# Kernel optimization log

Measured on AMD Instinct MI355X. Metric: run time of the kernel, lower is better.

Reference implementation:

```python
import jax, jax.numpy as jnp
import numpy as np

HIDDEN = 2048
NUM_ROUTED = 24          # num_routed_experts(6) * segmentation_factor(4)
ROUTED_INTER = 512       # intermediate_dim(2048) // segmentation_factor(4)
NUM_SHARED = 2
SHARED_INTER = 2048
TOP_K = 6


def setup_inputs() -> dict:
    key = jax.random.key(0)
    ks = jax.random.split(key, 8)
    std = 0.02
    x = jax.random.normal(ks[0], (2, 2048, HIDDEN), dtype=jnp.float32)
    gate_w = jax.random.normal(ks[1], (NUM_ROUTED, HIDDEN), dtype=jnp.float32) * (0.02 / np.sqrt(HIDDEN))
    shared_w1 = jax.random.normal(ks[2], (NUM_SHARED, HIDDEN, SHARED_INTER), dtype=jnp.float32) * std
    shared_w3 = jax.random.normal(ks[3], (NUM_SHARED, HIDDEN, SHARED_INTER), dtype=jnp.float32) * std
    shared_w2 = jax.random.normal(ks[4], (NUM_SHARED, SHARED_INTER, HIDDEN), dtype=jnp.float32) * std
    routed_w1 = jax.random.normal(ks[5], (NUM_ROUTED, HIDDEN, ROUTED_INTER), dtype=jnp.float32) * std
    routed_w3 = jax.random.normal(ks[6], (NUM_ROUTED, HIDDEN, ROUTED_INTER), dtype=jnp.float32) * std
    routed_w2 = jax.random.normal(ks[7], (NUM_ROUTED, ROUTED_INTER, HIDDEN), dtype=jnp.float32) * std
    return {"x": x, "gate_w": gate_w,
            "shared_w1": shared_w1, "shared_w2": shared_w2, "shared_w3": shared_w3,
            "routed_w1": routed_w1, "routed_w2": routed_w2, "routed_w3": routed_w3}


def _swiglu_ffn(x, w1, w2, w3):
    # x: [..., n, h]; w1,w3: [..., h, i]; w2: [..., i, h]  (dropout inactive at eval)
    h = jax.nn.silu(jnp.einsum('nh,ehi->eni', x, w1)) * jnp.einsum('nh,ehi->eni', x, w3)
    return jnp.einsum('eni,eih->enh', h, w2)


def reference(x, gate_w, shared_w1, shared_w2, shared_w3, routed_w1, routed_w2, routed_w3):
    B, S, H = x.shape
    x_flat = x.reshape(-1, H)                       # [N, H]
    N = x_flat.shape[0]

    # shared experts (summed)
    shared_out = _swiglu_ffn(x_flat, shared_w1, shared_w2, shared_w3).sum(axis=0)  # [N, H]

    # routing (eval mode: no bias added to logits, aux_loss = 0)
    scores = jax.nn.sigmoid(x_flat @ gate_w.T)      # [N, E]
    top_scores, top_idx = jax.lax.top_k(scores, TOP_K)
    top_weights = top_scores / (top_scores.sum(-1, keepdims=True) + 1e-9)  # [N, K]

    # dense dispatch/combine weights [N, E] (indices unique per row)
    dense_w = jnp.zeros((N, NUM_ROUTED), dtype=x.dtype)
    dense_w = dense_w.at[jnp.arange(N)[:, None], top_idx].set(top_weights)

    # run every routed expert on all tokens, combine with routing weights
    expert_out = _swiglu_ffn(x_flat, routed_w1, routed_w2, routed_w3)  # [E, N, H]
    combined = jnp.einsum('ne,enh->nh', dense_w, expert_out)

    output = (shared_out + combined).reshape(B, S, H)
    aux_loss = jnp.float32(0.0)  # eval mode
    return output, aux_loss
```

## Files before the change

### kernel.cpp

```cpp
#include <hip/hip_runtime.h>
#include <hip/hip_bf16.h>

#define HID   2048
#define NTOK  4096
#define NEXP  24
#define SHCOL 4096
#define TOPK  6
#define NSLOT (NTOK * TOPK)

typedef __bf16 bf16_t;
typedef __bf16 bf16x8 __attribute__((ext_vector_type(8)));
typedef __bf16 bf16x4 __attribute__((ext_vector_type(4)));
typedef float  f32x4  __attribute__((ext_vector_type(4)));

__device__ __forceinline__ void async_copy16(const bf16_t* g, bf16_t* l) {
  __builtin_amdgcn_global_load_lds(
      (const __attribute__((address_space(1))) unsigned int*)g,
      (__attribute__((address_space(3))) unsigned int*)l,
      16, 0, 0);
}
template<int N> __device__ __forceinline__ void wait_vm() {
  asm volatile("s_waitcnt vmcnt(%0)" :: "n"(N) : "memory");
}
__device__ __forceinline__ void memfence_sched() { asm volatile("" ::: "memory"); }

__device__ __forceinline__ bf16x8 frag32(const bf16_t* region, int row, int cc) {
  return *(const bf16x8*)(region + row * 32 + ((cc ^ ((row >> 1) & 3)) << 3));
}

__device__ __forceinline__ void tcast_tile(
    const float* __restrict__ src, bf16_t* __restrict__ dst,
    int C, long dstStride, int c0, int r0, int tid) {
  __shared__ float t[64][68];
  {
    const int tr = tid >> 4, tc = tid & 15;
#pragma unroll
    for (int p = 0; p < 4; ++p) {
      const int r = p * 16 + tr;
      const float4 v = *(const float4*)(src + (long)(r0 + r) * C + c0 + tc * 4);
      *(float4*)&t[r][tc * 4] = v;
    }
  }
  __syncthreads();
  {
    const int l8 = tid & 7, rb = l8 * 8;
#pragma unroll
    for (int p = 0; p < 2; ++p) {
      const int c = p * 32 + (tid >> 3);
      bf16x8 o;
#pragma unroll
      for (int s = 0; s < 8; ++s) o[s] = (bf16_t)t[rb + s][c];
      *(bf16x8*)(dst + (long)(c0 + c) * dstStride + r0 + rb) = o;
    }
  }
}

__global__ __launch_bounds__(256) void prep(
    const float* __restrict__ x, bf16_t* __restrict__ xb,
    const float* __restrict__ sw1, const float* __restrict__ rw1,
    const float* __restrict__ sw3, const float* __restrict__ rw3,
    const float* __restrict__ sw2, const float* __restrict__ rw2,
    bf16_t* __restrict__ w1t, bf16_t* __restrict__ w3t,
    bf16_t* __restrict__ w2ts, bf16_t* __restrict__ rw2t) {
  int bid = blockIdx.x;
  if (bid < 8192) {
    int i = bid * 256 + threadIdx.x;
    float4 v = ((const float4*)x)[i];
    bf16x4 o = { (bf16_t)v.x, (bf16_t)v.y, (bf16_t)v.z, (bf16_t)v.w };
    ((bf16x4*)xb)[i] = o;
    return;
  }
  bid -= 8192;
  const float* src; bf16_t* dst; int C; long dstStride, seS, deS; int BX, nPer;
  if (bid < 2048)       { src=sw1; dst=w1t;                  C=2048; dstStride=2048; seS=2048L*2048; deS=2048L*2048; BX=32; nPer=1024; }
  else if (bid < 8192)  { bid-=2048;  src=rw1; dst=w1t+(long)SHCOL*HID; C=512;  dstStride=2048; seS=2048L*512;  deS=512L*2048;  BX=8;  nPer=256; }
  else if (bid < 10240) { bid-=8192;  src=sw3; dst=w3t;                 C=2048; dstStride=2048; seS=2048L*2048; deS=2048L*2048; BX=32; nPer=1024; }
  else if (bid < 16384) { bid-=10240; src=rw3; dst=w3t+(long)SHCOL*HID; C=512;  dstStride=2048; seS=2048L*512;  deS=512L*2048;  BX=8;  nPer=256; }
  else if (bid < 18432) { bid-=16384; src=sw2; dst=w2ts;                C=2048; dstStride=4096; seS=2048L*2048; deS=2048;       BX=32; nPer=1024; }
  else                  { bid-=18432; src=rw2; dst=rw2t;                C=2048; dstStride=512;  seS=512L*2048;  deS=2048L*512;  BX=32; nPer=256; }
  const int e  = bid / nPer;
  const int rem = bid - e * nPer;
  const int by = rem / BX;
  const int bx = rem - by * BX;
  tcast_tile(src + (long)e * seS, dst + (long)e * deS, C, dstStride,
             bx * 64, by * 64, threadIdx.x);
}

__global__ void gate_topk(const float* __restrict__ x, const float* __restrict__ gw,
                          int* __restrict__ tk_idx, float* __restrict__ tk_w,
                          float* __restrict__ aux) {
  int lane = threadIdx.x & 63;
  int wave = threadIdx.x >> 6;
  int token = blockIdx.x * 4 + wave;
  const float* xr = x + (long)token * HID;
  float xv[32];
#pragma unroll
  for (int i = 0; i < 32; ++i) xv[i] = xr[lane + i * 64];
  float sc[NEXP];
#pragma unroll
  for (int e = 0; e < NEXP; ++e) {
    const float* g = gw + (long)e * HID;
    float s = 0.f;
#pragma unroll
    for (int i = 0; i < 32; ++i) s += xv[i] * g[lane + i * 64];
#pragma unroll
    for (int off = 32; off > 0; off >>= 1) s += __shfl_down(s, off);
    sc[e] = s;
  }
  if (lane == 0) {
    float sg[NEXP];
#pragma unroll
    for (int e = 0; e < NEXP; ++e) sg[e] = 1.0f / (1.0f + expf(-sc[e]));
    unsigned taken = 0;
    int   sel[TOPK];
    float sw[TOPK];
    float sum = 0.f;
    for (int k = 0; k < TOPK; ++k) {
      float best = -1.f; int bi = 0;
#pragma unroll
      for (int e = 0; e < NEXP; ++e) {
        bool avail = !(taken & (1u << e));
        if (avail && sg[e] > best) { best = sg[e]; bi = e; }
      }
      taken |= (1u << bi);
      sel[k] = bi; sw[k] = best; sum += best;
    }
    float inv = 1.0f / (sum + 1e-9f);
#pragma unroll
    for (int k = 0; k < TOPK; ++k) {
      tk_idx[token * TOPK + k] = sel[k];
      tk_w[token * TOPK + k]   = sw[k] * inv;
    }
  }
  if (blockIdx.x == 0 && threadIdx.x == 0) *aux = 0.0f;
}

__global__ void dispatch(const int* __restrict__ tk_idx, const float* __restrict__ tk_w,
                         int* __restrict__ perm, float* __restrict__ wslot,
                         int* __restrict__ slot_of, int* __restrict__ meta,
                         int* __restrict__ uptab, int* __restrict__ dntab) {
  __shared__ int cnt[NEXP], cnt2[NEXP], off[NEXP + 1];
  int tid = threadIdx.x;
  if (tid < NEXP) { cnt[tid] = 0; cnt2[tid] = 0; }
  __syncthreads();
  for (int i = tid; i < NSLOT; i += 1024) atomicAdd(&cnt[tk_idx[i]], 1);
  __syncthreads();
  if (tid == 0) {
    int o = 0, un = 0, dn = 0;
    for (int e = 0; e < NEXP; ++e) {
      off[e] = o;
      int c = cnt[e];
      for (int r0 = 0; r0 < c; r0 += 256) uptab[un++] = (e << 16) | r0;
      for (int r0 = 0; r0 < c; r0 += 128) dntab[dn++] = (e << 16) | r0;
      o += c;
    }
    off[NEXP] = o;
    meta[0] = un; meta[1] = dn;
    for (int e = 0; e < NEXP; ++e) { meta[8 + e] = cnt[e]; meta[32 + e] = off[e]; }
  }
  __syncthreads();
  for (int i = tid; i < NSLOT; i += 1024) {
    int e = tk_idx[i];
    int loc = atomicAdd(&cnt2[e], 1);
    int slot = off[e] + loc;
    perm[slot] = i / TOPK;
    wslot[slot] = tk_w[i];
    slot_of[i] = slot;
  }
}

__global__ __launch_bounds__(512, 2) void gemm_up(
    const bf16_t* __restrict__ xb, const bf16_t* __restrict__ w1t,
    const bf16_t* __restrict__ w3t, bf16_t* __restrict__ hsh,
    bf16_t* __restrict__ hr, const int* __restrict__ perm,
    const float* __restrict__ wslot, const int* __restrict__ meta,
    const int* __restrict__ uptab) {
  __shared__ bf16_t lds[4 * 16384];
  const int bid = blockIdx.x;
  const int tid  = threadIdx.x;
  const int lane = tid & 63;
  const int wave = tid >> 6;
  const int wm = wave >> 2;
  const int wc = wave & 3;
  const bool role_sh = bid < 512;
  int m0 = 0, j0 = 0, jc = 0, M = 256, bslot = 0;
  const bf16_t *b1G, *b3G;
  if (role_sh) {
    m0 = (bid >> 5) * 256; j0 = (bid & 31) * 128;
    b1G = w1t + (long)j0 * HID;
    b3G = w3t + (long)j0 * HID;
  } else {
    int t = bid - 512;
    int rt = t >> 2; jc = t & 3;
    if (rt >= meta[0]) return;
    int pk = uptab[rt];
    int e = pk >> 16, row0 = pk & 0xffff;
    bslot = meta[32 + e] + row0;
    M = min(256, meta[8 + e] - row0);
    int col = SHCOL + e * 512 + jc * 128;
    b1G = w1t + (long)col * HID;
    b3G = w3t + (long)col * HID;
  }
  const bf16_t* gsrc[4];
  int loff[4];
#pragma unroll
  for (int it = 0; it < 4; ++it) {
    int idx = it * 512 + tid;
    if (idx < 1024) {
      int r = idx >> 2, c = idx & 3;
      long rowbase;
      if (role_sh) rowbase = (long)(m0 + r) * HID;
      else         rowbase = (long)perm[bslot + ((r < M) ? r : 0)] * HID;
      gsrc[it] = xb + rowbase + ((c ^ ((r >> 1) & 3)) << 3);
      loff[it] = idx << 3;
    } else if (idx < 1536) {
      int i2 = idx - 1024; int r = i2 >> 2, c = i2 & 3;
      gsrc[it] = b1G + (long)r * HID + ((c ^ ((r >> 1) & 3)) << 3);
      loff[it] = 8192 + (i2 << 3);
    } else {
      int i2 = idx - 1536; int r = i2 >> 2, c = i2 & 3;
      gsrc[it] = b3G + (long)r * HID + ((c ^ ((r >> 1) & 3)) << 3);
      loff[it] = 12288 + (i2 << 3);
    }
  }
  auto STAGE = [&](int t) {
    bf16_t* sb = lds + (t & 3) * 16384;
#pragma unroll
    for (int it = 0; it < 4; ++it)
      async_copy16(gsrc[it] + t * 32, sb + loff[it]);
  };

  f32x4 acc1[8][2] = {};
  f32x4 acc3[8][2] = {};
  const int NT = HID / 32;
  const int rA = wm * 128 + (lane & 15);
  const int rB = wc * 32 + (lane & 15);
  const int cc = lane >> 4;
  STAGE(0); STAGE(1); STAGE(2);
  for (int t = 0; t < NT; ++t) {
    if (t + 2 < NT)      wait_vm<8>();
    else if (t + 1 < NT) wait_vm<4>();
    else                 wait_vm<0>();
    __builtin_amdgcn_s_barrier();
    memfence_sched();
    if (t + 3 < NT) STAGE(t + 3);
    const bf16_t* sb = lds + (t & 3) * 16384;
    bf16x8 a[8], b1[2], b3[2];
#pragma unroll
    for (int fm = 0; fm < 8; ++fm) a[fm] = frag32(sb, rA + fm * 16, cc);
#pragma unroll
    for (int fn = 0; fn < 2; ++fn) {
      b1[fn] = frag32(sb + 8192,  rB + fn * 16, cc);
      b3[fn] = frag32(sb + 12288, rB + fn * 16, cc);
    }
    __builtin_amdgcn_s_setprio(1);
#pragma unroll
    for (int fn = 0; fn < 2; ++fn)
#pragma unroll
      for (int fm = 0; fm < 8; ++fm) {
        acc1[fm][fn] = __builtin_amdgcn_mfma_f32_16x16x32_bf16(a[fm], b1[fn], acc1[fm][fn], 0, 0, 0);
        acc3[fm][fn] = __builtin_amdgcn_mfma_f32_16x16x32_bf16(a[fm], b3[fn], acc3[fm][fn], 0, 0, 0);
      }
    __builtin_amdgcn_s_setprio(0);
    memfence_sched();
  }
  const int mloc_base = wm * 128 + ((lane >> 4) << 2);
  const int cloc = wc * 32 + (lane & 15);
#pragma unroll
  for (int fm = 0; fm < 8; ++fm) {
#pragma unroll
    for (int jj = 0; jj < 4; ++jj) {
      const int mloc = mloc_base + fm * 16 + jj;
      if (role_sh) {
        bf16_t* dst = hsh + (long)(m0 + mloc) * SHCOL + j0 + cloc;
#pragma unroll
        for (int fn = 0; fn < 2; ++fn) {
          const float u1 = acc1[fm][fn][jj];
          const float u3 = acc3[fm][fn][jj];
          dst[fn * 16] = (bf16_t)((u1 / (1.0f + __expf(-u1))) * u3);
        }
      } else if (mloc < M) {
        const int slot = bslot + mloc;
        const float w = wslot[slot];
        bf16_t* dst = hr + (long)slot * 512 + jc * 128 + cloc;
#pragma unroll
        for (int fn = 0; fn < 2; ++fn) {
          const float u1 = acc1[fm][fn][jj];
          const float u3 = acc3[fm][fn][jj];
          dst[fn * 16] = (bf16_t)((u1 / (1.0f + __expf(-u1))) * u3 * w);
        }
      }
    }
  }
}

__global__ __launch_bounds__(512, 2) void gemm_down(
    const bf16_t* __restrict__ hsh, const bf16_t* __restrict__ w2ts,
    const bf16_t* __restrict__ hr, const bf16_t* __restrict__ rw2t,
    float* __restrict__ sout, bf16_t* __restrict__ y,
    const int* __restrict__ meta, const int* __restrict__ dntab) {
  __shared__ bf16_t lds[3 * 12288];
  const int bid = blockIdx.x;
  const int tid  = threadIdx.x;
  const int lane = tid & 63;
  const int wave = tid >> 6;
  const int wm = wave >> 2;
  const int wc = wave & 3;
  const bool role_sh = bid < 256;
  int m0 = 0, n0, M = 128, bslot = 0, NT;
  const bf16_t *aG, *bG;
  long lda, ldb;
  if (role_sh) {
    m0 = (bid >> 3) * 128; n0 = (bid & 7) * 256;
    aG = hsh + (long)m0 * SHCOL; lda = SHCOL;
    bG = w2ts + (long)n0 * SHCOL; ldb = SHCOL;
    NT = SHCOL / 32;
  } else {
    int t = bid - 256;
    int rt = t >> 3; n0 = (t & 7) * 256;
    if (rt >= meta[1]) return;
    int pk = dntab[rt];
    int e = pk >> 16, row0 = pk & 0xffff;
    bslot = meta[32 + e] + row0;
    M = min(128, meta[8 + e] - row0);
    aG = hr + (long)bslot * 512; lda = 512;
    bG = rw2t + (long)e * (2048L * 512) + (long)n0 * 512; ldb = 512;
    NT = 512 / 32;
  }
  const bf16_t* gsrc[3];
  int loff[3];
#pragma unroll
  for (int it = 0; it < 3; ++it) {
    int idx = it * 512 + tid;
    if (idx < 512) {
      int r = idx >> 2, c = idx & 3;
      gsrc[it] = aG + (long)r * lda + ((c ^ ((r >> 1) & 3)) << 3);
      loff[it] = idx << 3;
    } else {
      int i2 = idx - 512; int r = i2 >> 2, c = i2 & 3;
      gsrc[it] = bG + (long)r * ldb + ((c ^ ((r >> 1) & 3)) << 3);
      loff[it] = 4096 + (i2 << 3);
    }
  }
  auto STAGE = [&](int t) {
    bf16_t* sb = lds + (t % 3) * 12288;
#pragma unroll
    for (int it = 0; it < 3; ++it)
      async_copy16(gsrc[it] + t * 32, sb + loff[it]);
  };

  f32x4 acc[4][4] = {};
  const int rA = wm * 64 + (lane & 15);
  const int rB = wc * 64 + (lane & 15);
  const int cc = lane >> 4;
  STAGE(0); STAGE(1);
  for (int t = 0; t < NT; ++t) {
    if (t + 1 < NT) wait_vm<3>();
    else            wait_vm<0>();
    __builtin_amdgcn_s_barrier();
    memfence_sched();
    if (t + 2 < NT) STAGE(t + 2);
    const bf16_t* sb = lds + (t % 3) * 12288;
    bf16x8 a[4], b[4];
#pragma unroll
    for (int fm = 0; fm < 4; ++fm) a[fm] = frag32(sb, rA + fm * 16, cc);
#pragma unroll
    for (int fn = 0; fn < 4; ++fn) b[fn] = frag32(sb + 4096, rB + fn * 16, cc);
    __builtin_amdgcn_s_setprio(1);
#pragma unroll
    for (int fn = 0; fn < 4; ++fn)
#pragma unroll
      for (int fm = 0; fm < 4; ++fm)
        acc[fm][fn] = __builtin_amdgcn_mfma_f32_16x16x32_bf16(a[fm], b[fn], acc[fm][fn], 0, 0, 0);
    __builtin_amdgcn_s_setprio(0);
    memfence_sched();
  }
  const int mloc_base = wm * 64 + ((lane >> 4) << 2);
  const int cbase = n0 + wc * 64 + (lane & 15);
#pragma unroll
  for (int fm = 0; fm < 4; ++fm)
#pragma unroll
    for (int jj = 0; jj < 4; ++jj) {
      const int mloc = mloc_base + fm * 16 + jj;
      if (role_sh) {
#pragma unroll
        for (int fn = 0; fn < 4; ++fn)
          sout[(long)(m0 + mloc) * HID + cbase + fn * 16] = acc[fm][fn][jj];
      } else if (mloc < M) {
#pragma unroll
        for (int fn = 0; fn < 4; ++fn)
          y[(long)(bslot + mloc) * HID + cbase + fn * 16] = (bf16_t)acc[fm][fn][jj];
      }
    }
}

__global__ void combine(const float* __restrict__ sout, const bf16_t* __restrict__ y,
                        const int* __restrict__ slot_of, float* __restrict__ out) {
  const int n = blockIdx.x;
  const int c0 = threadIdx.x * 8;
  float acc[8];
  const float4* sp = (const float4*)(sout + (long)n * HID + c0);
  float4 s0 = sp[0], s1 = sp[1];
  acc[0]=s0.x; acc[1]=s0.y; acc[2]=s0.z; acc[3]=s0.w;
  acc[4]=s1.x; acc[5]=s1.y; acc[6]=s1.z; acc[7]=s1.w;
#pragma unroll
  for (int k = 0; k < TOPK; ++k) {
    int slot = slot_of[n * TOPK + k];
    bf16x8 v = *(const bf16x8*)(y + (long)slot * HID + c0);
#pragma unroll
    for (int i = 0; i < 8; ++i) acc[i] += (float)v[i];
  }
  float4* op = (float4*)(out + (long)n * HID + c0);
  op[0] = make_float4(acc[0], acc[1], acc[2], acc[3]);
  op[1] = make_float4(acc[4], acc[5], acc[6], acc[7]);
}

__global__ void fill_sentinel(float* out, int n) {
  for (int i = blockIdx.x * 256 + threadIdx.x; i < n; i += gridDim.x * 256)
    out[i] = 12345.0f;
}

extern "C" void kernel_launch(void* const* d_in, const int* in_sizes, int n_in,
                              void* d_out, int out_size, void* d_ws, size_t ws_size,
                              hipStream_t stream) {
  (void)in_sizes; (void)n_in;
  const float* x   = (const float*)d_in[0];
  const float* gw  = (const float*)d_in[1];
  const float* sw1 = (const float*)d_in[2];
  const float* sw2 = (const float*)d_in[3];
  const float* sw3 = (const float*)d_in[4];
  const float* rw1 = (const float*)d_in[5];
  const float* rw2 = (const float*)d_in[6];
  const float* rw3 = (const float*)d_in[7];
  float* out = (float*)d_out;

  const size_t OFF_XB    = 0;
  const size_t OFF_W1T   = 16777216;
  const size_t OFF_W3T   = 83886080;
  const size_t OFF_W2TS  = 150994944;
  const size_t OFF_RW2T  = 167772160;
  const size_t OFF_HSH   = 218103808;
  const size_t OFF_HR    = 251658240;
  const size_t OFF_SOUT  = 277086208;
  const size_t OFF_TKI   = 310640640;
  const size_t OFF_TKW   = 310738944;
  const size_t OFF_PERM  = 310837248;
  const size_t OFF_WSLOT = 310935552;
  const size_t OFF_SLOTOF= 311033856;
  const size_t OFF_META  = 311132160;
  const size_t OFF_UPTAB = 311136256;
  const size_t OFF_DNTAB = 311140352;
  const size_t NEED      = 311148544;
  if (ws_size < NEED) {
    fill_sentinel<<<4096, 256, 0, stream>>>(out, out_size);
    return;
  }
  char* ws = (char*)d_ws;
  bf16_t* xb     = (bf16_t*)(ws + OFF_XB);
  bf16_t* w1t    = (bf16_t*)(ws + OFF_W1T);
  bf16_t* w3t    = (bf16_t*)(ws + OFF_W3T);
  bf16_t* w2ts   = (bf16_t*)(ws + OFF_W2TS);
  bf16_t* rw2t   = (bf16_t*)(ws + OFF_RW2T);
  bf16_t* hsh    = (bf16_t*)(ws + OFF_HSH);
  bf16_t* hr     = (bf16_t*)(ws + OFF_HR);
  float*  sout   = (float*)(ws + OFF_SOUT);
  bf16_t* y      = (bf16_t*)(ws + OFF_W1T);
  int*    tki    = (int*)(ws + OFF_TKI);
  float*  tkw    = (float*)(ws + OFF_TKW);
  int*    perm   = (int*)(ws + OFF_PERM);
  float*  wslot  = (float*)(ws + OFF_WSLOT);
  int*    slotof = (int*)(ws + OFF_SLOTOF);
  int*    meta   = (int*)(ws + OFF_META);
  int*    uptab  = (int*)(ws + OFF_UPTAB);
  int*    dntab  = (int*)(ws + OFF_DNTAB);

  gate_topk<<<1024, 256, 0, stream>>>(x, gw, tki, tkw, out + (size_t)NTOK * HID);
  dispatch<<<1, 1024, 0, stream>>>(tki, tkw, perm, wslot, slotof, meta, uptab, dntab);
  prep<<<32768, 256, 0, stream>>>(x, xb, sw1, rw1, sw3, rw3, sw2, rw2,
                                  w1t, w3t, w2ts, rw2t);

  gemm_up<<<dim3(512 + 480), 512, 0, stream>>>(xb, w1t, w3t, hsh, hr, perm, wslot, meta, uptab);
  gemm_down<<<dim3(256 + 1728), 512, 0, stream>>>(hsh, w2ts, hr, rw2t, sout, y, meta, dntab);
  combine<<<dim3(NTOK), 256, 0, stream>>>(sout, y, slotof, out);
}
```

Before: 649.0 us.

## Restructure gemm_up main loop into BK=64 double-buffered, phased MFMA schedule

Reworks the up-projection GEMM loop from a 4-stage BK=32 ring to a 2-buffer BK=64 scheme with a new XOR swizzle for 64-wide rows. Each k-step is split into four MFMA phases separated by barriers, and the global-to-LDS loads for the next tiles are issued between phases so they overlap compute. Occupancy hint drops to 1 block per CU because fewer fragment registers are live per phase. This aims to cut barrier count per k and improve latency hiding, but it adds many more barriers inside each step and carries a risk of buffer hazards when the next tile is loaded into a buffer that is still being read.

```diff
diff --git a/kernel.cpp b/kernel.cpp
--- a/kernel.cpp
+++ b/kernel.cpp
@@ -23,9 +23,15 @@
   asm volatile("s_waitcnt vmcnt(%0)" :: "n"(N) : "memory");
 }
 __device__ __forceinline__ void memfence_sched() { asm volatile("" ::: "memory"); }
+__device__ __forceinline__ void barp() {
+  memfence_sched(); __builtin_amdgcn_s_barrier(); memfence_sched();
+}
 
 __device__ __forceinline__ bf16x8 frag32(const bf16_t* region, int row, int cc) {
   return *(const bf16x8*)(region + row * 32 + ((cc ^ ((row >> 1) & 3)) << 3));
+}
+__device__ __forceinline__ bf16x8 frag64(const bf16_t* region, int row, int c8) {
+  return *(const bf16x8*)(region + row * 64 + ((c8 ^ (row & 7)) << 3));
 }
 
 __device__ __forceinline__ void tcast_tile(
@@ -169,13 +175,13 @@
   }
 }
 
-__global__ __launch_bounds__(512, 2) void gemm_up(
+__global__ __launch_bounds__(512, 1) void gemm_up(
     const bf16_t* __restrict__ xb, const bf16_t* __restrict__ w1t,
     const bf16_t* __restrict__ w3t, bf16_t* __restrict__ hsh,
     bf16_t* __restrict__ hr, const int* __restrict__ perm,
     const float* __restrict__ wslot, const int* __restrict__ meta,
     const int* __restrict__ uptab) {
-  __shared__ bf16_t lds[4 * 16384];
+  __shared__ bf16_t lds[2 * 32768];
   const int bid = blockIdx.x;
   const int tid  = threadIdx.x;
   const int lane = tid & 63;
@@ -201,66 +207,115 @@
     b1G = w1t + (long)col * HID;
     b3G = w3t + (long)col * HID;
   }
-  const bf16_t* gsrc[4];
-  int loff[4];
-#pragma unroll
-  for (int it = 0; it < 4; ++it) {
-    int idx = it * 512 + tid;
-    if (idx < 1024) {
-      int r = idx >> 2, c = idx & 3;
-      long rowbase;
-      if (role_sh) rowbase = (long)(m0 + r) * HID;
-      else         rowbase = (long)perm[bslot + ((r < M) ? r : 0)] * HID;
-      gsrc[it] = xb + rowbase + ((c ^ ((r >> 1) & 3)) << 3);
-      loff[it] = idx << 3;
-    } else if (idx < 1536) {
-      int i2 = idx - 1024; int r = i2 >> 2, c = i2 & 3;
-      gsrc[it] = b1G + (long)r * HID + ((c ^ ((r >> 1) & 3)) << 3);
-      loff[it] = 8192 + (i2 << 3);
+  const bf16_t* hsrc[4][2];
+  int hloff[4][2];
+#pragma unroll
+  for (int it = 0; it < 2; ++it) {
+    const int idx = it * 512 + tid;
+    const int r = idx >> 3;
+    const int c = idx & 7;
+    const int cs = c ^ (r & 7);
+    long rowA0, rowA1;
+    if (role_sh) {
+      rowA0 = (long)(m0 + r) * HID;
+      rowA1 = (long)(m0 + 128 + r) * HID;
     } else {
-      int i2 = idx - 1536; int r = i2 >> 2, c = i2 & 3;
-      gsrc[it] = b3G + (long)r * HID + ((c ^ ((r >> 1) & 3)) << 3);
-      loff[it] = 12288 + (i2 << 3);
-    }
-  }
-  auto STAGE = [&](int t) {
-    bf16_t* sb = lds + (t & 3) * 16384;
-#pragma unroll
-    for (int it = 0; it < 4; ++it)
-      async_copy16(gsrc[it] + t * 32, sb + loff[it]);
+      rowA0 = (long)perm[bslot + ((r < M) ? r : 0)] * HID;
+      rowA1 = (long)perm[bslot + ((128 + r < M) ? 128 + r : 0)] * HID;
+    }
+    hsrc[0][it] = xb + rowA0 + cs * 8;          hloff[0][it] = idx * 8;
+    hsrc[1][it] = xb + rowA1 + cs * 8;          hloff[1][it] = 8192 + idx * 8;
+    hsrc[2][it] = b1G + (long)r * HID + cs * 8; hloff[2][it] = 16384 + idx * 8;
+    hsrc[3][it] = b3G + (long)r * HID + cs * 8; hloff[3][it] = 24576 + idx * 8;
+  }
+  auto SH = [&](int t, int h) {
+    bf16_t* sb = lds + (t & 1) * 32768;
+    async_copy16(hsrc[h][0] + t * 64, sb + hloff[h][0]);
+    async_copy16(hsrc[h][1] + t * 64, sb + hloff[h][1]);
   };
 
   f32x4 acc1[8][2] = {};
   f32x4 acc3[8][2] = {};
-  const int NT = HID / 32;
-  const int rA = wm * 128 + (lane & 15);
-  const int rB = wc * 32 + (lane & 15);
-  const int cc = lane >> 4;
-  STAGE(0); STAGE(1); STAGE(2);
+  const int NT = HID / 64;
+  const int lrow = lane & 15;
+  const int lk   = lane >> 4;
+  SH(0, 0); SH(0, 1); SH(0, 2); SH(0, 3);
+  if (NT > 1) { SH(1, 0); SH(1, 1); SH(1, 2); }
+
   for (int t = 0; t < NT; ++t) {
-    if (t + 2 < NT)      wait_vm<8>();
-    else if (t + 1 < NT) wait_vm<4>();
-    else                 wait_vm<0>();
-    __builtin_amdgcn_s_barrier();
-    memfence_sched();
-    if (t + 3 < NT) STAGE(t + 3);
-    const bf16_t* sb = lds + (t & 3) * 16384;
-    bf16x8 a[8], b1[2], b3[2];
-#pragma unroll
-    for (int fm = 0; fm < 8; ++fm) a[fm] = frag32(sb, rA + fm * 16, cc);
-#pragma unroll
-    for (int fn = 0; fn < 2; ++fn) {
-      b1[fn] = frag32(sb + 8192,  rB + fn * 16, cc);
-      b3[fn] = frag32(sb + 12288, rB + fn * 16, cc);
-    }
+    if (t + 1 < NT) wait_vm<6>();
+    else            wait_vm<0>();
+    barp();
+    const bf16_t* sb  = lds + (t & 1) * 32768;
+    const bf16_t* aR  = sb + wm * 8192;
+    const bf16_t* b1R = sb + 16384;
+    const bf16_t* b3R = sb + 24576;
+    bf16x8 a[4][2], b1f[2][2], b3f[2][2];
+#pragma unroll
+    for (int fm = 0; fm < 4; ++fm)
+#pragma unroll
+      for (int kk = 0; kk < 2; ++kk)
+        a[fm][kk] = frag64(aR, fm * 16 + lrow, kk * 4 + lk);
+#pragma unroll
+    for (int fn = 0; fn < 2; ++fn)
+#pragma unroll
+      for (int kk = 0; kk < 2; ++kk)
+        b1f[fn][kk] = frag64(b1R, wc * 32 + fn * 16 + lrow, kk * 4 + lk);
+    if (t + 1 < NT) SH(t + 1, 3);
+    barp();
     __builtin_amdgcn_s_setprio(1);
 #pragma unroll
+    for (int kk = 0; kk < 2; ++kk)
+#pragma unroll
+      for (int fn = 0; fn < 2; ++fn)
+#pragma unroll
+        for (int fm = 0; fm < 4; ++fm)
+          acc1[fm][fn] = __builtin_amdgcn_mfma_f32_16x16x32_bf16(a[fm][kk], b1f[fn][kk], acc1[fm][fn], 0, 0, 0);
+    __builtin_amdgcn_s_setprio(0);
+    barp();
+#pragma unroll
     for (int fn = 0; fn < 2; ++fn)
 #pragma unroll
-      for (int fm = 0; fm < 8; ++fm) {
-        acc1[fm][fn] = __builtin_amdgcn_mfma_f32_16x16x32_bf16(a[fm], b1[fn], acc1[fm][fn], 0, 0, 0);
-        acc3[fm][fn] = __builtin_amdgcn_mfma_f32_16x16x32_bf16(a[fm], b3[fn], acc3[fm][fn], 0, 0, 0);
-      }
+      for (int kk = 0; kk < 2; ++kk)
+        b3f[fn][kk] = frag64(b3R, wc * 32 + fn * 16 + lrow, kk * 4 + lk);
+    if (t + 2 < NT) SH(t + 2, 2);
+    barp();
+    __builtin_amdgcn_s_setprio(1);
+#pragma unroll
+    for (int kk = 0; kk < 2; ++kk)
+#pragma unroll
+      for (int fn = 0; fn < 2; ++fn)
+#pragma unroll
+        for (int fm = 0; fm < 4; ++fm)
+          acc3[fm][fn] = __builtin_amdgcn_mfma_f32_16x16x32_bf16(a[fm][kk], b3f[fn][kk], acc3[fm][fn], 0, 0, 0);
+    __builtin_amdgcn_s_setprio(0);
+    barp();
+#pragma unroll
+    for (int fm = 0; fm < 4; ++fm)
+#pragma unroll
+      for (int kk = 0; kk < 2; ++kk)
+        a[fm][kk] = frag64(aR, 64 + fm * 16 + lrow, kk * 4 + lk);
+    barp();
+    __builtin_amdgcn_s_setprio(1);
+#pragma unroll
+    for (int kk = 0; kk < 2; ++kk)
+#pragma unroll
+      for (int fn = 0; fn < 2; ++fn)
+#pragma unroll
+        for (int fm = 0; fm < 4; ++fm)
+          acc1[4 + fm][fn] = __builtin_amdgcn_mfma_f32_16x16x32_bf16(a[fm][kk], b1f[fn][kk], acc1[4 + fm][fn], 0, 0, 0);
+    __builtin_amdgcn_s_setprio(0);
+    barp();
+    if (t + 2 < NT) { SH(t + 2, 0); SH(t + 2, 1); }
+    barp();
+    __builtin_amdgcn_s_setprio(1);
+#pragma unroll
+    for (int kk = 0; kk < 2; ++kk)
+#pragma unroll
+      for (int fn = 0; fn < 2; ++fn)
+#pragma unroll
+        for (int fm = 0; fm < 4; ++fm)
+          acc3[4 + fm][fn] = __builtin_amdgcn_mfma_f32_16x16x32_bf16(a[fm][kk], b3f[fn][kk], acc3[4 + fm][fn], 0, 0, 0);
     __builtin_amdgcn_s_setprio(0);
     memfence_sched();
   }
```

Result: no change. 636.6 us (-1.9%).
